# Kernel tuning notes

Hardware: AMD Instinct MI355X
Metric: run time of the kernel (lower is better)

The kernel has to match this reference:

```python
import jax, jax.numpy as jnp
import numpy as np

N, D, H1, K = 4096, 128, 256, 128


def setup_inputs() -> dict:
    key = jax.random.key(0)
    ks = jax.random.split(key, 8)
    A = jax.random.uniform(ks[3], (D, D), dtype=jnp.float32)
    A = A * (1.0 - jnp.eye(D, dtype=jnp.float32))  # DAG prob mask, no self-loops
    return {
        "x": jax.random.normal(ks[0], (N, D), dtype=jnp.float32),
        "weight": jax.random.normal(ks[1], (D, D), dtype=jnp.float32) * 0.1,
        "bias": jax.random.normal(ks[2], (1, D), dtype=jnp.float32) * 0.1,
        "A": A,
        "W1": jax.random.normal(ks[4], (D, H1), dtype=jnp.float32) * 0.1,
        "b1": jax.random.normal(ks[5], (H1,), dtype=jnp.float32) * 0.1,
        "W2": jax.random.normal(ks[6], (H1, K), dtype=jnp.float32) * 0.1,
        "b2": jax.random.normal(ks[7], (K,), dtype=jnp.float32) * 0.1,
    }


def reference(x, weight, bias, A, W1, b1, W2, b2):
    # to_adj (eval path): masked weights
    W = weight * A                                   # [D, D]
    y = x @ W + bias                                 # [N, D]
    # __expand__ builds diag(y[n]) [N,D,D]; since e[n,i,:] = y[n,i]*I[i,:],
    # the first Linear collapses to a per-row scaling of W1 (same math, fused):
    # e @ W1 -> y[n,i] * W1[i,:]
    h1 = jax.nn.relu(y[:, :, None] * W1[None, :, :] + b1)   # [N, D, H1]
    f = (h1 @ W2 + b2).sum(axis=2)                   # [N, D] (sum over output dim)
    # h_func, method='gnn'
    I = jnp.eye(D, dtype=x.dtype)
    A2 = jnp.square(W)
    M = I + A2 / D
    E = jnp.linalg.matrix_power(M, D - 1)
    h_val = (E.T * M).sum() - D
    # l1_reg (same prob mask in eval)
    reg = jnp.abs(W).sum()
    return (f, h_val, reg)
```

## Files before the change

kernel.cpp:

```cpp
#include <hip/hip_runtime.h>

#define NN 4096
#define DD 128
#define HH1 256

#define WS_S    0
#define WS_S2   16384
#define WS_S3   32768
#define WS_S4   49152
#define WS_W    65536
#define WS_W2S  81920
#define WS_PAIR 82176
#define WS_B2S  82688
#define WS_TACC 82696
#define WS_DONE 82708
#define WS_REGP 82712
#define WS_WT   82944
#define WS_XT   99328
#define WS_TH   623616
#define WS_A    656384
#define WS_B    689280
#define WS_REQ_FLOATS 722176
#define WS_REQ_BYTES  (WS_REQ_FLOATS * 4UL)

#define O_S    0
#define O_S2   16384
#define O_S3   32768
#define O_S4   49152
#define O_W2S  65536
#define O_B2S  65792
#define O_TACC 65808
#define O_DONE 65824
#define O_REGP 65840

__device__ __forceinline__ float waveReduce(float v) {
#pragma unroll
  for (int off = 32; off > 0; off >>= 1) v += __shfl_down(v, off, 64);
  return v;
}


__global__ __launch_bounds__(256) void kA3(
    const float* __restrict__ weight, const float* __restrict__ Amat,
    const float* __restrict__ W2, const float* __restrict__ b2,
    const float* __restrict__ b1v, const float* __restrict__ x,
    const float* __restrict__ W1, float* __restrict__ ws) {
  const int b = blockIdx.x, tid = threadIdx.x;
  __shared__ float s_lds[DD * DD];
  if (b < 64) {
    const float4* w4 = (const float4*)weight;
    const float4* a4 = (const float4*)Amat;
    float4* s4 = (float4*)s_lds;
    const float inv = 1.0f / 128.0f;
    for (int e = tid; e < DD * DD / 4; e += 256) {
      float4 wv = w4[e], av = a4[e], o;
      float t;
      t = wv.x * av.x; o.x = t * t * inv;
      t = wv.y * av.y; o.y = t * t * inv;
      t = wv.z * av.z; o.z = t * t * inv;
      t = wv.w * av.w; o.w = t * t * inv;
      s4[e] = o;
    }
    __syncthreads();
    const int i = (b << 1) + (tid >> 7), j = tid & 127;
    const float* row = &s_lds[i * DD];
    float acc = 0.f;
#pragma unroll 8
    for (int k = 0; k < DD; ++k) acc = fmaf(row[k], s_lds[k * DD + j], acc);
    ws[WS_S2 + i * DD + j] = acc;
  } else if (b < 72) {
    const int base = (b - 64) * 2048;
    const float inv = 1.0f / 128.0f;
    for (int e = tid; e < 2048; e += 256) {
      const int idx = base + e;
      const float w = weight[idx] * Amat[idx];
      const int k = idx >> 7, i = idx & 127;
      ws[WS_W + idx] = w;
      ws[WS_WT + i * DD + k] = w;
      ws[WS_S + idx] = w * w * inv;
    }
  } else if (b == 72) {
    __shared__ float red[4];
    float v = (tid < 128) ? b2[tid] : 0.f;
    v = waveReduce(v);
    if ((tid & 63) == 0) red[tid >> 6] = v;
    __syncthreads();
    if (tid == 0) ws[WS_B2S] = (red[0] + red[1]) + (red[2] + red[3]);
    if (tid >= 64 && tid < 74) ws[WS_TACC + (tid - 64)] = 0.f;
    if (tid == 96) *(unsigned int*)(ws + WS_DONE) = 0u;
  } else if (b < 81) {
    const int bb = b - 73;
    const int base = bb * 2048;
    float s = 0.f;
    for (int e = tid; e < 2048; e += 256) {
      const int idx = base + e;
      s += fabsf(weight[idx] * Amat[idx]);
    }
    s = waveReduce(s);
    __shared__ float red2[4];
    if ((tid & 63) == 0) red2[tid >> 6] = s;
    __syncthreads();
    if (tid == 0) ws[WS_REGP + bb] = (red2[0] + red2[1]) + (red2[2] + red2[3]);
  } else if (b < 145) {
    float* xs = s_lds;
    const int n0 = (b - 81) * 64;
    const float4* x4 = (const float4*)x;
    for (int e = tid; e < 2048; e += 256) {
      const int r = e >> 5, c = e & 31;
      const float4 v = x4[(n0 + r) * 32 + c];
      float* p = &xs[r * 133 + (c << 2)];
      p[0] = v.x; p[1] = v.y; p[2] = v.z; p[3] = v.w;
    }
    __syncthreads();
    float* xT = ws + WS_XT;
    const int c = tid & 15, ks = tid >> 4;
#pragma unroll
    for (int m = 0; m < 8; ++m) {
      const int k = ks + (m << 4);
      float4 o;
      o.x = xs[((c << 2) + 0) * 133 + k];
      o.y = xs[((c << 2) + 1) * 133 + k];
      o.z = xs[((c << 2) + 2) * 133 + k];
      o.w = xs[((c << 2) + 3) * 133 + k];
      *(float4*)&xT[k * NN + n0 + (c << 2)] = o;
    }
  } else {
    const int i = b - 145;
    float* kT = s_lds;
    float* kS = s_lds + 256;
    float* kC = s_lds + 512;
    __shared__ float redb[8];
    __shared__ float base2[2];
    const int j = tid;
    const float4* r = (const float4*)(W2 + j * 128);
    float4 s4v = make_float4(0.f, 0.f, 0.f, 0.f);
#pragma unroll 8
    for (int k = 0; k < 32; ++k) {
      const float4 v = r[k];
      s4v.x += v.x; s4v.y += v.y; s4v.z += v.z; s4v.w += v.w;
    }
    const float w2s = (s4v.x + s4v.y) + (s4v.z + s4v.w);
    const float w = W1[i * HH1 + j];
    const float bj = b1v[j];
    const float s = w * w2s, c = bj * w2s;
    float th, ds, dc, bs, bc;
    if (w > 0.f) {
      th = -bj / w; ds = s; dc = c; bs = 0.f; bc = 0.f;
    } else if (w < 0.f) {
      th = -bj / w; ds = -s; dc = -c; bs = s; bc = c;
    } else {
      th = 3.4e38f; ds = 0.f; dc = 0.f; bs = 0.f; bc = fmaxf(bj, 0.f) * w2s;
    }
    {
      const float rs = waveReduce(bs), rc = waveReduce(bc);
      if ((tid & 63) == 0) {
        redb[tid >> 6] = rs;
        redb[4 + (tid >> 6)] = rc;
      }
    }
    kT[tid] = th; kS[tid] = ds; kC[tid] = dc;
    __syncthreads();
    if (tid == 0) {
      base2[0] = (redb[0] + redb[1]) + (redb[2] + redb[3]);
      base2[1] = (redb[4] + redb[5]) + (redb[6] + redb[7]);
    }
    for (int kk = 2; kk <= 256; kk <<= 1) {
      for (int jj = kk >> 1; jj > 0; jj >>= 1) {
        __syncthreads();
        const int ixj = tid ^ jj;
        if (ixj > tid) {
          const bool up = ((tid & kk) == 0);
          const float ta = kT[tid], tb = kT[ixj];
          if ((ta > tb) == up) {
            kT[tid] = tb; kT[ixj] = ta;
            const float sa = kS[tid], sb = kS[ixj];
            kS[tid] = sb; kS[ixj] = sa;
            const float ca = kC[tid], cb = kC[ixj];
            kC[tid] = cb; kC[ixj] = ca;
          }
        }
      }
    }
    __syncthreads();
    for (int off = 1; off < 256; off <<= 1) {
      float vs = 0.f, vc = 0.f;
      if (tid >= off) { vs = kS[tid - off]; vc = kC[tid - off]; }
      __syncthreads();
      kS[tid] += vs; kC[tid] += vc;
      __syncthreads();
    }
    const float b_s = base2[0], b_c = base2[1];
    ws[WS_TH + i * 256 + tid] = kT[tid];
    ws[WS_A + i * 257 + tid + 1] = b_s + kS[tid];
    ws[WS_B + i * 257 + tid + 1] = b_c + kC[tid];
    if (tid == 0) {
      ws[WS_A + i * 257] = b_s;
      ws[WS_B + i * 257] = b_c;
    }
  }
}

__global__ __launch_bounds__(256) void kS34(float* __restrict__ ws) {
  const int tid = threadIdx.x;
  const int sb = blockIdx.x;
  const bool isS4 = sb >= 64;
  const int mb = isS4 ? sb - 64 : sb;
  const float* __restrict__ L = ws + WS_S2;
  const float* __restrict__ R = ws + (isS4 ? WS_S2 : WS_S);
  float* __restrict__ O = ws + (isS4 ? WS_S4 : WS_S3);
  const int i = (mb << 1) + (tid >> 7), j = tid & 127;
  float acc = 0.f;
#pragma unroll 8
  for (int k = 0; k < DD; ++k) acc = fmaf(L[i * DD + k], R[k * DD + j], acc);
  O[i * DD + j] = acc;
}

__global__ __launch_bounds__(256) void kC6(const float* __restrict__ bias,
                                           float* __restrict__ ws,
                                           float* __restrict__ out) {
  const int tid = threadIdx.x;
  if (blockIdx.x < 512) {
    __shared__ float lT[4 * 256];
    __shared__ float lA[4 * 257];
    __shared__ float lB[4 * 257];
    __shared__ float ts[256 * 5];
    const int fb = blockIdx.x;
    const int n0 = (fb >> 5) << 8, i0 = (fb & 31) << 2;
    const int w = tid >> 6, l = tid & 63;
    const int iu = __builtin_amdgcn_readfirstlane(i0 + w);

#pragma unroll
    for (int q = 0; q < 4; ++q) {
      lT[(q << 8) + tid] = ws[WS_TH + (i0 + q) * 256 + tid];
      lA[q * 257 + tid] = ws[WS_A + (i0 + q) * 257 + tid];
      lB[q * 257 + tid] = ws[WS_B + (i0 + q) * 257 + tid];
      if (tid == 0) {
        lA[q * 257 + 256] = ws[WS_A + (i0 + q) * 257 + 256];
        lB[q * 257 + 256] = ws[WS_B + (i0 + q) * 257 + 256];
      }
    }

    const float* __restrict__ xT = ws + WS_XT;
    const float* __restrict__ wr = ws + WS_WT + iu * DD;
    float t[4] = {0.f, 0.f, 0.f, 0.f};
#pragma unroll 8
    for (int k = 0; k < DD; ++k) {
      const float wv = wr[k];
      const float4 xv = *(const float4*)&xT[k * NN + n0 + (l << 2)];
      t[0] = fmaf(xv.x, wv, t[0]);
      t[1] = fmaf(xv.y, wv, t[1]);
      t[2] = fmaf(xv.z, wv, t[2]);
      t[3] = fmaf(xv.w, wv, t[3]);
    }
    const float bv = bias[iu];
    const float sb2 = ws[WS_B2S];
    __syncthreads();

    const float* Tw = &lT[w << 8];
    const float* Aw = &lA[w * 257];
    const float* Bw = &lB[w * 257];
#pragma unroll
    for (int q = 0; q < 4; ++q) {
      const float yq = t[q] + bv;
      int m = 0;
#pragma unroll
      for (int st = 128; st > 0; st >>= 1) {
        if (Tw[m + st - 1] <= yq) m += st;
      }
      const float f = fmaf(Aw[m], yq, Bw[m]) + sb2;
      ts[((l << 2) + q) * 5 + w] = f;
    }
    __syncthreads();
    const int m = tid;
    float4 o;
    o.x = ts[m * 5 + 0]; o.y = ts[m * 5 + 1];
    o.z = ts[m * 5 + 2]; o.w = ts[m * 5 + 3];
    *(float4*)&out[(n0 + m) * DD + i0] = o;
    return;
  }
  const int tb = blockIdx.x - 512;
  const int i = (tb << 1) + (tid >> 7), j = tid & 127;
  const float* S1 = ws + WS_S;
  const float* S2 = ws + WS_S2;
  const float* S3 = ws + WS_S3;
  const float* S4 = ws + WS_S4;
  const float a1 = S1[i * DD + j], a2 = S2[i * DD + j], a3 = S3[i * DD + j];
  const float b1t = S1[j * DD + i], b2t = S2[j * DD + i],
              b3t = S3[j * DD + i], b4t = S4[j * DD + i];
  float e7 = 0.f;
#pragma unroll 8
  for (int k = 0; k < DD; ++k) e7 = fmaf(S3[i * DD + k], S4[k * DD + j], e7);
  float c[10];
  c[0] = a1 * b1t; c[1] = a2 * b1t; c[2] = a2 * b2t; c[3] = a3 * b2t;
  c[4] = a3 * b3t; c[5] = a3 * b4t; c[6] = e7 * b1t; c[7] = e7 * b2t;
  c[8] = e7 * b3t; c[9] = e7 * b4t;
  __shared__ float red[4][10];
#pragma unroll
  for (int m = 0; m < 10; ++m) {
    const float v = waveReduce(c[m]);
    if ((tid & 63) == 0) red[tid >> 6][m] = v;
  }
  __syncthreads();
  if (tid == 0) {
    float* tacc = ws + WS_TACC;
    for (int m = 0; m < 10; ++m)
      atomicAdd(&tacc[m], (red[0][m] + red[1][m]) + (red[2][m] + red[3][m]));
    __threadfence();
    unsigned int* done = (unsigned int*)(ws + WS_DONE);
    const unsigned int old = atomicAdd(done, 1u);
    if (old == 63u) {
      __threadfence();
      double h = 0.0, C = 8128.0;
      for (int kk = 2; kk <= 11; ++kk) {
        const float tv = atomicAdd(&tacc[kk - 2], 0.0f);
        h += C * (double)tv;
        C = C * (double)(128 - kk) / (double)(kk + 1);
      }
      float reg = 0.f;
      for (int m = 0; m < 8; ++m) reg += ws[WS_REGP + m];
      out[NN * DD] = (float)h;
      out[NN * DD + 1] = reg;
    }
  }
}

__global__ __launch_bounds__(256) void kA_old(
    const float* __restrict__ weight, const float* __restrict__ Amat,
    const float* __restrict__ W2, const float* __restrict__ b2,
    float* __restrict__ ws) {
  const int b = blockIdx.x, tid = threadIdx.x;
  if (b < 64) {
    __shared__ float s_lds[DD * DD];
    const float4* w4 = (const float4*)weight;
    const float4* a4 = (const float4*)Amat;
    float4* s4 = (float4*)s_lds;
    const float inv = 1.0f / 128.0f;
    for (int e = tid; e < DD * DD / 4; e += 256) {
      float4 wv = w4[e], av = a4[e], o;
      float t;
      t = wv.x * av.x; o.x = t * t * inv;
      t = wv.y * av.y; o.y = t * t * inv;
      t = wv.z * av.z; o.z = t * t * inv;
      t = wv.w * av.w; o.w = t * t * inv;
      s4[e] = o;
    }
    __syncthreads();
    const int i = (b << 1) + (tid >> 7), j = tid & 127;
    const float* row = &s_lds[i * DD];
    float acc = 0.f;
#pragma unroll 8
    for (int k = 0; k < DD; ++k) acc = fmaf(row[k], s_lds[k * DD + j], acc);
    ws[O_S2 + i * DD + j] = acc;
  } else if (b < 72) {
    const int base = (b - 64) * 2048;
    const float inv = 1.0f / 128.0f;
    for (int e = tid; e < 2048; e += 256) {
      const int idx = base + e;
      const float w = weight[idx] * Amat[idx];
      ws[O_S + idx] = w * w * inv;
    }
  } else if (b == 72) {
    const float4* r = (const float4*)(W2 + tid * 128);
    float4 s4 = make_float4(0.f, 0.f, 0.f, 0.f);
#pragma unroll 8
    for (int k = 0; k < 32; ++k) {
      const float4 v = r[k];
      s4.x += v.x; s4.y += v.y; s4.z += v.z; s4.w += v.w;
    }
    ws[O_W2S + tid] = (s4.x + s4.y) + (s4.z + s4.w);
  } else if (b == 73) {
    __shared__ float red[4];
    float v = (tid < 128) ? b2[tid] : 0.f;
    v = waveReduce(v);
    if ((tid & 63) == 0) red[tid >> 6] = v;
    __syncthreads();
    if (tid == 0) ws[O_B2S] = (red[0] + red[1]) + (red[2] + red[3]);
    if (tid >= 64 && tid < 74) ws[O_TACC + (tid - 64)] = 0.f;
    if (tid == 96) *(unsigned int*)(ws + O_DONE) = 0u;
  } else {
    const int bb = b - 74;
    const int base = bb * 2048;
    float s = 0.f;
    for (int e = tid; e < 2048; e += 256) {
      const int idx = base + e;
      s += fabsf(weight[idx] * Amat[idx]);
    }
    s = waveReduce(s);
    __shared__ float red[4];
    if ((tid & 63) == 0) red[tid >> 6] = s;
    __syncthreads();
    if (tid == 0) ws[O_REGP + bb] = (red[0] + red[1]) + (red[2] + red[3]);
  }
}

__global__ __launch_bounds__(256) void kB_old(
    const float* __restrict__ x, const float* __restrict__ weight,
    const float* __restrict__ Amat, const float* __restrict__ bias,
    const float* __restrict__ W1, const float* __restrict__ b1v,
    float* __restrict__ ws, float* __restrict__ out) {
  const int tid = threadIdx.x;
  if (blockIdx.x < 128) {
    const int sb = blockIdx.x;
    const bool isS4 = sb >= 64;
    const int mb = isS4 ? sb - 64 : sb;
    const float* __restrict__ L = ws + O_S2;
    const float* __restrict__ R = ws + (isS4 ? O_S2 : O_S);
    float* __restrict__ O = ws + (isS4 ? O_S4 : O_S3);
    const int i = (mb << 1) + (tid >> 7), j = tid & 127;
    float acc = 0.f;
#pragma unroll 8
    for (int k = 0; k < DD; ++k) acc = fmaf(L[i * DD + k], R[k * DD + j], acc);
    O[i * DD + j] = acc;
    return;
  }
  __shared__ float xs[64 * 132];
  __shared__ float4 fq[4 * 256];
  __shared__ float wcol[4 * 128];
  __shared__ float ts[64 * 5];
  const int fb = blockIdx.x - 128;
  const int i0 = (fb & 31) << 2, n0 = (fb >> 5) << 6;
  const float4* x4 = (const float4*)x;
  for (int e = tid; e < 64 * 32; e += 256) {
    const int r = e >> 5, c = e & 31;
    *(float4*)&xs[r * 132 + (c << 2)] = x4[(n0 + r) * 32 + c];
  }
  for (int e = tid; e < 512; e += 256) {
    const int w = e >> 7, k = e & 127;
    const int gi = k * DD + i0 + w;
    wcol[(w << 7) + k] = weight[gi] * Amat[gi];
  }
  const float* w2s = ws + O_W2S;
  for (int e = tid; e < 1024; e += 256) {
    const int w = e >> 8, j = e & 255;
    fq[(w << 8) + j] = make_float4(W1[(i0 + w) * HH1 + j], b1v[j], w2s[j], 0.f);
  }
  __syncthreads();
  const int w = tid >> 6, l = tid & 63;
  float t = bias[i0 + w];
  const float4* xr = (const float4*)&xs[l * 132];
  const float4* wc = (const float4*)&wcol[w << 7];
#pragma unroll
  for (int k = 0; k < 32; ++k) {
    const float4 xv = xr[k], wv = wc[k];
    t = fmaf(xv.x, wv.x, t);
    t = fmaf(xv.y, wv.y, t);
    t = fmaf(xv.z, wv.z, t);
    t = fmaf(xv.w, wv.w, t);
  }
  float acc = ws[O_B2S];
  const float4* fp = &fq[w << 8];
#pragma unroll 8
  for (int j = 0; j < HH1; ++j) {
    const float4 c = fp[j];
    acc = fmaf(fmaxf(fmaf(t, c.x, c.y), 0.f), c.z, acc);
  }
  ts[l * 5 + w] = acc;
  __syncthreads();
  if (tid < 64) {
    const float4 o = make_float4(ts[tid * 5 + 0], ts[tid * 5 + 1],
                                 ts[tid * 5 + 2], ts[tid * 5 + 3]);
    *(float4*)&out[(n0 + tid) * DD + i0] = o;
  }
}

__global__ __launch_bounds__(256) void kC_old(float* __restrict__ ws,
                                              float* __restrict__ out) {
  const int tid = threadIdx.x;
  const int i = (blockIdx.x << 1) + (tid >> 7), j = tid & 127;
  const float* S1 = ws + O_S;
  const float* S2 = ws + O_S2;
  const float* S3 = ws + O_S3;
  const float* S4 = ws + O_S4;
  const float a1 = S1[i * DD + j], a2 = S2[i * DD + j], a3 = S3[i * DD + j];
  const float b1t = S1[j * DD + i], b2t = S2[j * DD + i],
              b3t = S3[j * DD + i], b4t = S4[j * DD + i];
  float e7 = 0.f;
#pragma unroll 8
  for (int k = 0; k < DD; ++k) e7 = fmaf(S3[i * DD + k], S4[k * DD + j], e7);
  float c[10];
  c[0] = a1 * b1t; c[1] = a2 * b1t; c[2] = a2 * b2t; c[3] = a3 * b2t;
  c[4] = a3 * b3t; c[5] = a3 * b4t; c[6] = e7 * b1t; c[7] = e7 * b2t;
  c[8] = e7 * b3t; c[9] = e7 * b4t;
  __shared__ float red[4][10];
#pragma unroll
  for (int m = 0; m < 10; ++m) {
    const float v = waveReduce(c[m]);
    if ((tid & 63) == 0) red[tid >> 6][m] = v;
  }
  __syncthreads();
  if (tid == 0) {
    float* tacc = ws + O_TACC;
    for (int m = 0; m < 10; ++m)
      atomicAdd(&tacc[m], (red[0][m] + red[1][m]) + (red[2][m] + red[3][m]));
    __threadfence();
    unsigned int* done = (unsigned int*)(ws + O_DONE);
    const unsigned int old = atomicAdd(done, 1u);
    if (old == 63u) {
      __threadfence();
      double h = 0.0, C = 8128.0;
      for (int kk = 2; kk <= 11; ++kk) {
        const float tv = atomicAdd(&tacc[kk - 2], 0.0f);
        h += C * (double)tv;
        C = C * (double)(128 - kk) / (double)(kk + 1);
      }
      float reg = 0.f;
      for (int m = 0; m < 8; ++m) reg += ws[O_REGP + m];
      out[NN * DD] = (float)h;
      out[NN * DD + 1] = reg;
    }
  }
}

extern "C" void kernel_launch(void* const* d_in, const int* in_sizes, int n_in,
                              void* d_out, int out_size, void* d_ws,
                              size_t ws_size, hipStream_t stream) {
  const float* x      = (const float*)d_in[0];
  const float* weight = (const float*)d_in[1];
  const float* bias   = (const float*)d_in[2];
  const float* Amat   = (const float*)d_in[3];
  const float* W1     = (const float*)d_in[4];
  const float* b1v    = (const float*)d_in[5];
  const float* W2     = (const float*)d_in[6];
  const float* b2     = (const float*)d_in[7];
  float* out = (float*)d_out;
  float* ws  = (float*)d_ws;

  if (ws_size >= WS_REQ_BYTES) {
    kA3<<<273, 256, 0, stream>>>(weight, Amat, W2, b2, b1v, x, W1, ws);
    kS34<<<128, 256, 0, stream>>>(ws);
    kC6<<<576, 256, 0, stream>>>(bias, ws, out);
  } else {
    kA_old<<<82, 256, 0, stream>>>(weight, Amat, W2, b2, ws);
    kB_old<<<128 + 2048, 256, 0, stream>>>(x, weight, Amat, bias, W1, b1v, ws,
                                           out);
    kC_old<<<64, 256, 0, stream>>>(ws, out);
  }
}
```

Before: 124.3 us.

## Move y=xW GEMM into middle kernel and replace bitonic sort with rank counting

The x@W product moves out of the final kernel into a new middle kernel. There it runs alongside the S3/S4 matrix products and writes a transposed y buffer, so the final kernel only loads y and does the breakpoint lookup. The per-column breakpoint table build moves from the first kernel to the middle one. Its bitonic sort plus prefix scan is replaced by an O(256) rank-count loop per thread with no barriers. This rebalances work across the three launches and cuts many barriers. In exchange it adds a workspace round-trip for y and needs a larger workspace, so a too-small workspace would fall back to the old path.

```diff
diff --git a/kernel.cpp b/kernel.cpp
--- a/kernel.cpp
+++ b/kernel.cpp
@@ -9,18 +9,16 @@
 #define WS_S3   32768
 #define WS_S4   49152
 #define WS_W    65536
-#define WS_W2S  81920
-#define WS_PAIR 82176
 #define WS_B2S  82688
 #define WS_TACC 82696
 #define WS_DONE 82708
 #define WS_REGP 82712
-#define WS_WT   82944
 #define WS_XT   99328
 #define WS_TH   623616
 #define WS_A    656384
 #define WS_B    689280
-#define WS_REQ_FLOATS 722176
+#define WS_YT   722176
+#define WS_REQ_FLOATS 1246464
 #define WS_REQ_BYTES  (WS_REQ_FLOATS * 4UL)
 
 #define O_S    0
@@ -40,11 +38,10 @@
 }
 
 
-__global__ __launch_bounds__(256) void kA3(
+__global__ __launch_bounds__(256) void kA4(
     const float* __restrict__ weight, const float* __restrict__ Amat,
-    const float* __restrict__ W2, const float* __restrict__ b2,
-    const float* __restrict__ b1v, const float* __restrict__ x,
-    const float* __restrict__ W1, float* __restrict__ ws) {
+    const float* __restrict__ b2, const float* __restrict__ x,
+    float* __restrict__ ws) {
   const int b = blockIdx.x, tid = threadIdx.x;
   __shared__ float s_lds[DD * DD];
   if (b < 64) {
@@ -74,9 +71,7 @@
     for (int e = tid; e < 2048; e += 256) {
       const int idx = base + e;
       const float w = weight[idx] * Amat[idx];
-      const int k = idx >> 7, i = idx & 127;
       ws[WS_W + idx] = w;
-      ws[WS_WT + i * DD + k] = w;
       ws[WS_S + idx] = w * w * inv;
     }
   } else if (b == 72) {
@@ -101,7 +96,7 @@
     if ((tid & 63) == 0) red2[tid >> 6] = s;
     __syncthreads();
     if (tid == 0) ws[WS_REGP + bb] = (red2[0] + red2[1]) + (red2[2] + red2[3]);
-  } else if (b < 145) {
+  } else {
     float* xs = s_lds;
     const int n0 = (b - 81) * 64;
     const float4* x4 = (const float4*)x;
@@ -124,99 +119,106 @@
       o.w = xs[((c << 2) + 3) * 133 + k];
       *(float4*)&xT[k * NN + n0 + (c << 2)] = o;
     }
+  }
+}
+
+__global__ __launch_bounds__(256) void kB5(const float* __restrict__ bias,
+                                           const float* __restrict__ W1,
+                                           const float* __restrict__ b1v,
+                                           const float* __restrict__ W2,
+                                           float* __restrict__ ws) {
+  const int tid = threadIdx.x;
+  if (blockIdx.x < 128) {
+    const int sb = blockIdx.x;
+    const bool isS4 = sb >= 64;
+    const int mb = isS4 ? sb - 64 : sb;
+    const float* __restrict__ L = ws + WS_S2;
+    const float* __restrict__ R = ws + (isS4 ? WS_S2 : WS_S);
+    float* __restrict__ O = ws + (isS4 ? WS_S4 : WS_S3);
+    const int i = (mb << 1) + (tid >> 7), j = tid & 127;
+    float acc = 0.f;
+#pragma unroll 8
+    for (int k = 0; k < DD; ++k) acc = fmaf(L[i * DD + k], R[k * DD + j], acc);
+    O[i * DD + j] = acc;
+    return;
+  }
+  if (blockIdx.x < 384) {
+    const int kb = blockIdx.x - 128;
+    const int n0 = (kb & 15) << 8, i0 = (kb >> 4) << 3;
+    const int n = n0 + tid;
+    const float* __restrict__ xT = ws + WS_XT;
+    const float* __restrict__ Wm = ws + WS_W;
+    float* __restrict__ yT = ws + WS_YT;
+    float acc[8];
+#pragma unroll
+    for (int q = 0; q < 8; ++q) acc[q] = 0.f;
+#pragma unroll 8
+    for (int k = 0; k < DD; ++k) {
+      const float xv = xT[k * NN + n];
+      const float* Wk = Wm + k * DD + i0;
+#pragma unroll
+      for (int q = 0; q < 8; ++q) acc[q] = fmaf(Wk[q], xv, acc[q]);
+    }
+#pragma unroll
+    for (int q = 0; q < 8; ++q) yT[(i0 + q) * NN + n] = acc[q] + bias[i0 + q];
+    return;
+  }
+  const int i = blockIdx.x - 384;
+  __shared__ float kT[256], kS[256], kC[256];
+  __shared__ float redb[8];
+  const int j = tid;
+  const float4* r = (const float4*)(W2 + j * 128);
+  float4 s4v = make_float4(0.f, 0.f, 0.f, 0.f);
+#pragma unroll 8
+  for (int k = 0; k < 32; ++k) {
+    const float4 v = r[k];
+    s4v.x += v.x; s4v.y += v.y; s4v.z += v.z; s4v.w += v.w;
+  }
+  const float w2s = (s4v.x + s4v.y) + (s4v.z + s4v.w);
+  const float w = W1[i * HH1 + j];
+  const float bj = b1v[j];
+  const float s = w * w2s, c = bj * w2s;
+  float th, ds, dc, bs, bc;
+  if (w > 0.f) {
+    th = -bj / w; ds = s; dc = c; bs = 0.f; bc = 0.f;
+  } else if (w < 0.f) {
+    th = -bj / w; ds = -s; dc = -c; bs = s; bc = c;
   } else {
-    const int i = b - 145;
-    float* kT = s_lds;
-    float* kS = s_lds + 256;
-    float* kC = s_lds + 512;
-    __shared__ float redb[8];
-    __shared__ float base2[2];
-    const int j = tid;
-    const float4* r = (const float4*)(W2 + j * 128);
-    float4 s4v = make_float4(0.f, 0.f, 0.f, 0.f);
-#pragma unroll 8
-    for (int k = 0; k < 32; ++k) {
-      const float4 v = r[k];
-      s4v.x += v.x; s4v.y += v.y; s4v.z += v.z; s4v.w += v.w;
-    }
-    const float w2s = (s4v.x + s4v.y) + (s4v.z + s4v.w);
-    const float w = W1[i * HH1 + j];
-    const float bj = b1v[j];
-    const float s = w * w2s, c = bj * w2s;
-    float th, ds, dc, bs, bc;
-    if (w > 0.f) {
-      th = -bj / w; ds = s; dc = c; bs = 0.f; bc = 0.f;
-    } else if (w < 0.f) {
-      th = -bj / w; ds = -s; dc = -c; bs = s; bc = c;
-    } else {
-      th = 3.4e38f; ds = 0.f; dc = 0.f; bs = 0.f; bc = fmaxf(bj, 0.f) * w2s;
-    }
-    {
-      const float rs = waveReduce(bs), rc = waveReduce(bc);
-      if ((tid & 63) == 0) {
-        redb[tid >> 6] = rs;
-        redb[4 + (tid >> 6)] = rc;
-      }
-    }
-    kT[tid] = th; kS[tid] = ds; kC[tid] = dc;
-    __syncthreads();
-    if (tid == 0) {
-      base2[0] = (redb[0] + redb[1]) + (redb[2] + redb[3]);
-      base2[1] = (redb[4] + redb[5]) + (redb[6] + redb[7]);
-    }
-    for (int kk = 2; kk <= 256; kk <<= 1) {
-      for (int jj = kk >> 1; jj > 0; jj >>= 1) {
-        __syncthreads();
-        const int ixj = tid ^ jj;
-        if (ixj > tid) {
-          const bool up = ((tid & kk) == 0);
-          const float ta = kT[tid], tb = kT[ixj];
-          if ((ta > tb) == up) {
-            kT[tid] = tb; kT[ixj] = ta;
-            const float sa = kS[tid], sb = kS[ixj];
-            kS[tid] = sb; kS[ixj] = sa;
-            const float ca = kC[tid], cb = kC[ixj];
-            kC[tid] = cb; kC[ixj] = ca;
-          }
-        }
-      }
-    }
-    __syncthreads();
-    for (int off = 1; off < 256; off <<= 1) {
-      float vs = 0.f, vc = 0.f;
-      if (tid >= off) { vs = kS[tid - off]; vc = kC[tid - off]; }
-      __syncthreads();
-      kS[tid] += vs; kC[tid] += vc;
-      __syncthreads();
-    }
-    const float b_s = base2[0], b_c = base2[1];
-    ws[WS_TH + i * 256 + tid] = kT[tid];
-    ws[WS_A + i * 257 + tid + 1] = b_s + kS[tid];
-    ws[WS_B + i * 257 + tid + 1] = b_c + kC[tid];
-    if (tid == 0) {
-      ws[WS_A + i * 257] = b_s;
-      ws[WS_B + i * 257] = b_c;
-    }
-  }
-}
-
-__global__ __launch_bounds__(256) void kS34(float* __restrict__ ws) {
-  const int tid = threadIdx.x;
-  const int sb = blockIdx.x;
-  const bool isS4 = sb >= 64;
-  const int mb = isS4 ? sb - 64 : sb;
-  const float* __restrict__ L = ws + WS_S2;
-  const float* __restrict__ R = ws + (isS4 ? WS_S2 : WS_S);
-  float* __restrict__ O = ws + (isS4 ? WS_S4 : WS_S3);
-  const int i = (mb << 1) + (tid >> 7), j = tid & 127;
-  float acc = 0.f;
-#pragma unroll 8
-  for (int k = 0; k < DD; ++k) acc = fmaf(L[i * DD + k], R[k * DD + j], acc);
-  O[i * DD + j] = acc;
-}
-
-__global__ __launch_bounds__(256) void kC6(const float* __restrict__ bias,
-                                           float* __restrict__ ws,
+    th = 3.4e38f; ds = 0.f; dc = 0.f; bs = 0.f; bc = fmaxf(bj, 0.f) * w2s;
+  }
+  {
+    const float rs = waveReduce(bs), rc = waveReduce(bc);
+    if ((tid & 63) == 0) {
+      redb[tid >> 6] = rs;
+      redb[4 + (tid >> 6)] = rc;
+    }
+  }
+  kT[tid] = th; kS[tid] = ds; kC[tid] = dc;
+  __syncthreads();
+  const float b_s = (redb[0] + redb[1]) + (redb[2] + redb[3]);
+  const float b_c = (redb[4] + redb[5]) + (redb[6] + redb[7]);
+  int rank = 0;
+  float accS = 0.f, accC = 0.f;
+  for (int jj = 0; jj < 256; ++jj) {
+    const float thj = kT[jj];
+    const float dsj = kS[jj], dcj = kC[jj];
+    const bool le = (thj < th) || (thj == th && jj <= j);
+    if (le) {
+      ++rank;
+      accS += dsj;
+      accC += dcj;
+    }
+  }
+  ws[WS_TH + i * 256 + (rank - 1)] = th;
+  ws[WS_A + i * 257 + rank] = b_s + accS;
+  ws[WS_B + i * 257 + rank] = b_c + accC;
+  if (tid == 0) {
+    ws[WS_A + i * 257] = b_s;
+    ws[WS_B + i * 257] = b_c;
+  }
+}
+
+__global__ __launch_bounds__(256) void kC7(float* __restrict__ ws,
                                            float* __restrict__ out) {
   const int tid = threadIdx.x;
   if (blockIdx.x < 512) {
@@ -239,29 +241,18 @@
         lB[q * 257 + 256] = ws[WS_B + (i0 + q) * 257 + 256];
       }
     }
-
-    const float* __restrict__ xT = ws + WS_XT;
-    const float* __restrict__ wr = ws + WS_WT + iu * DD;
-    float t[4] = {0.f, 0.f, 0.f, 0.f};
-#pragma unroll 8
-    for (int k = 0; k < DD; ++k) {
-      const float wv = wr[k];
-      const float4 xv = *(const float4*)&xT[k * NN + n0 + (l << 2)];
-      t[0] = fmaf(xv.x, wv, t[0]);
-      t[1] = fmaf(xv.y, wv, t[1]);
-      t[2] = fmaf(xv.z, wv, t[2]);
-      t[3] = fmaf(xv.w, wv, t[3]);
-    }
-    const float bv = bias[iu];
+    const float* __restrict__ yT = ws + WS_YT;
+    const float4 yv = *(const float4*)&yT[iu * NN + n0 + (l << 2)];
     const float sb2 = ws[WS_B2S];
     __syncthreads();
 
     const float* Tw = &lT[w << 8];
     const float* Aw = &lA[w * 257];
     const float* Bw = &lB[w * 257];
+    const float yq4[4] = {yv.x, yv.y, yv.z, yv.w};
 #pragma unroll
     for (int q = 0; q < 4; ++q) {
-      const float yq = t[q] + bv;
+      const float yq = yq4[q];
       int m = 0;
 #pragma unroll
       for (int st = 128; st > 0; st >>= 1) {
@@ -526,9 +517,9 @@
   float* ws  = (float*)d_ws;
 
   if (ws_size >= WS_REQ_BYTES) {
-    kA3<<<273, 256, 0, stream>>>(weight, Amat, W2, b2, b1v, x, W1, ws);
-    kS34<<<128, 256, 0, stream>>>(ws);
-    kC6<<<576, 256, 0, stream>>>(bias, ws, out);
+    kA4<<<145, 256, 0, stream>>>(weight, Amat, b2, x, ws);
+    kB5<<<512, 256, 0, stream>>>(bias, W1, b1v, W2, ws);
+    kC7<<<576, 256, 0, stream>>>(ws, out);
   } else {
     kA_old<<<82, 256, 0, stream>>>(weight, Amat, W2, b2, ws);
     kB_old<<<128 + 2048, 256, 0, stream>>>(x, weight, Amat, bias, W1, b1v, ws,
```

Result: faster. 120.2 us (-3.3%).
